# Optimization experiments

Measured on AMD Instinct MI355X. Metric: run time of the kernel, lower is better.

The kernel has to match this reference:

```python
import jax, jax.numpy as jnp
import numpy as np
from jax import lax

B, HI, WI, D = 8, 64, 64, 128
HO, WO = HI // 2, WI // 2
N_IN, N_OUT = HI * WI, HO * WO
NUM_ITERS = 3
EPS = 1e-6


def _build_indices(Ho, Wo):
    # replicates _build_q_and_in_idx: per coarse position, 9 relative offsets
    dys = np.repeat(np.arange(-1, 2), 3)
    dxs = np.tile(np.arange(-1, 2), 3)
    oy = np.arange(Ho)[:, None, None]
    ox = np.arange(Wo)[None, :, None]
    ny = oy + dys
    nx = ox + dxs
    valid = (ny >= 0) & (ny < Ho) & (nx >= 0) & (nx < Wo)  # (Ho,Wo,9)
    coarse = np.where(valid, ny * Wo + nx, 0)
    base = (oy * Wo + ox) * 9
    g9 = np.where(valid, base + np.arange(9), 0).reshape(-1, 9)
    c9 = coarse.reshape(-1, 9)
    q_idx = np.stack([np.tile(g9, (1, 4))] * 4)
    col_idx = np.stack([np.tile(c9, (1, 4))] * 4)
    in_idx = np.stack([np.tile(np.where(valid, coarse * 4 + h, 0).reshape(-1, 9), (1, 4)) for h in range(4)])
    return q_idx.astype(np.int32), in_idx.astype(np.int32), col_idx.astype(np.int32)


Q_IDX, IN_IDX, COL_IDX = _build_indices(HO, WO)
# NATTEN kernel-3 neighborhoods: window center clamped to stay in-bounds.
NY = np.clip(np.arange(HO) - 1, 0, HO - 3)[:, None] + np.arange(3)  # (HO,3)
NX = np.clip(np.arange(WO) - 1, 0, WO - 3)[:, None] + np.arange(3)  # (WO,3)


def _ln(x, g, b, eps=1e-5):
    mu = x.mean(-1, keepdims=True)
    var = ((x - mu) ** 2).mean(-1, keepdims=True)
    return (x - mu) * lax.rsqrt(var + eps) * g + b


def _forward(x, seed_w, wq, wk, wv, w1, b1, w2, b2, ln_in_g, ln_in_b, ln_out_g, ln_out_b, rpb, tau):
    ny, nx = jnp.asarray(NY), jnp.asarray(NX)
    q_idx = jnp.asarray(Q_IDX)

    def unfold(t):  # (B,HI,WI,D) -> (B,4,HO,WO,D); head = ky*2+kx (F.unfold order)
        return t.reshape(B, HO, 2, WO, 2, D).transpose(0, 2, 4, 1, 3, 5).reshape(B, 4, HO, WO, D)

    k = unfold((_ln(x, ln_in_g, ln_in_b) @ wk.T).reshape(B, HI, WI, D))
    v = unfold((x @ wv.T).reshape(B, HI, WI, D))
    k_n = k[:, :, ny][:, :, :, :, nx]  # (B,4,HO,3,WO,3,D)
    v_n = v[:, :, ny][:, :, :, :, nx]

    x_map = x.reshape(B, HI, WI, D).transpose(0, 3, 1, 2)
    seed = lax.conv_general_dilated(x_map, seed_w, (2, 2), ((1, 1), (1, 1)),
                                    dimension_numbers=('NCHW', 'OIHW', 'NCHW'))
    x_out = _ln(seed.reshape(B, D, N_OUT).transpose(0, 2, 1), ln_out_g, ln_out_b)

    scale = jnp.exp(tau)
    attn36 = a_col_h = None
    for _ in range(NUM_ITERS):
        q = (_ln(x_out, ln_out_g, ln_out_b) @ wq.T).reshape(B, HO, WO, D)
        # na2d_qk (q broadcast over the 4 heads) + relative position bias
        logits = jnp.einsum('byxd,bhykxld->bhyxkl', q, k_n).reshape(B, 4, HO, WO, 9) + rpb.reshape(1, 4, 1, 1, 9)
        attn = jax.nn.softmax(logits * scale, axis=-1) + EPS
        flat = attn.reshape(B, 4, N_OUT * 9)
        attn36 = jnp.take_along_axis(
            flat, jnp.broadcast_to(q_idx.reshape(1, 4, -1), (B, 4, N_OUT * 36)), axis=-1
        ).reshape(B, 4, N_OUT, 36)
        a_col_h = attn36 / (attn36.sum(axis=(1, 3), keepdims=True) + EPS)
        attn9 = a_col_h[..., :9].reshape(B, 4, HO, WO, 3, 3)
        # na2d_av then sum over heads
        updates = jnp.einsum('bhyxkl,bhykxld->byxd', attn9, v_n).reshape(B, N_OUT, D)
        x_out = x_out + updates
        h1 = jax.nn.gelu(x_out @ w1.T + b1, approximate=False)
        x_out = x_out + _ln(h1 @ w2.T + b2, ln_out_g, ln_out_b)
    return x_out, attn36, a_col_h


def setup_inputs() -> dict:
    key = jax.random.key(0)
    ks = jax.random.split(key, 8)
    n = lambda k, shape, s: jax.random.normal(k, shape, jnp.float32) * s
    D2 = 2 * D
    return {
        'x': jax.random.normal(ks[0], (B, N_IN, D), jnp.float32),
        'seed_w': n(ks[1], (D, D, 3, 3), (2.0 / (9 * D)) ** 0.5),
        'wq': n(ks[2], (D, D), D ** -0.5),
        'wk': n(ks[3], (D, D), D ** -0.5),
        'wv': n(ks[4], (D, D), D ** -0.5),
        'w1': n(ks[5], (D2, D), D ** -0.5),
        'b1': jnp.zeros((D2,), jnp.float32),
        'w2': n(ks[6], (D, D2), D2 ** -0.5),
        'b2': jnp.zeros((D,), jnp.float32),
        'ln_in_g': jnp.ones((D,), jnp.float32),
        'ln_in_b': jnp.zeros((D,), jnp.float32),
        'ln_out_g': jnp.ones((D,), jnp.float32),
        'ln_out_b': jnp.zeros((D,), jnp.float32),
        'rpb': n(ks[7], (4, 9), 0.02),
        'tau': jnp.float32(np.log(D ** -0.5)),
    }


def reference(x, seed_w, wq, wk, wv, w1, b1, w2, b2, ln_in_g, ln_in_b, ln_out_g, ln_out_b, rpb, tau):
    x_out, attn36, a_col_h = _forward(x, seed_w, wq, wk, wv, w1, b1, w2, b2,
                                      ln_in_g, ln_in_b, ln_out_g, ln_out_b, rpb, tau)
    # A_col: scatter_add over dim 1 -> A_col[b, in_idx[i,j], j] += a_col_h[b,i,j]
    rows = jnp.asarray(IN_IDX).reshape(4 * N_OUT, 36)
    cols = jnp.broadcast_to(jnp.arange(36), rows.shape)
    A_col = jnp.zeros((B, N_IN, N_OUT), x.dtype).at[:, rows, cols].add(a_col_h.reshape(B, 4 * N_OUT, 36))
    # A_row: scatter_add over dim 2 -> A_row[b, i, col_idx[i,j]] += attn36[b,i,j]
    ri = jnp.broadcast_to(jnp.arange(4 * N_OUT)[:, None], (4 * N_OUT, 36))
    A_row = jnp.zeros((B, N_IN, N_OUT), x.dtype).at[:, ri, jnp.asarray(COL_IDX).reshape(4 * N_OUT, 36)].add(
        attn36.reshape(B, 4 * N_OUT, 36))
    return x_out, A_row, A_col
```

## Files before the change

### kernel.cpp

```cpp
#include <hip/hip_runtime.h>
#include <hip/hip_bf16.h>
#include <math.h>

#define BB   8
#define HI_  64
#define WI_  64
#define DD   128
#define HO_  32
#define WO_  32
#define NIN  4096
#define NOUT 1024
#define LN_EPS 1e-5f
#define ATT_EPS 1e-6f

typedef short bf16x8 __attribute__((ext_vector_type(8)));
typedef float f32x4  __attribute__((ext_vector_type(4)));

__device__ __forceinline__ ushort f2bf(float f) {
    union { float f; unsigned u; } a; a.f = f;
    unsigned u = a.u;
    return (ushort)((u + 0x7FFFu + ((u >> 16) & 1u)) >> 16);
}
__device__ __forceinline__ float bf2f(ushort u) {
    union { unsigned u; float f; } a; a.u = ((unsigned)u) << 16;
    return a.f;
}

__global__ __launch_bounds__(256)
void wconvert_kernel(const float* __restrict__ wq, const float* __restrict__ wk,
                     const float* __restrict__ wv, const float* __restrict__ w1,
                     const float* __restrict__ w2, const float* __restrict__ sw,
                     ushort* __restrict__ dst)
{
    int i = blockIdx.x * 256 + threadIdx.x;
    float v;
    if (i < 16384)        v = wk[i];
    else if (i < 32768)   v = wv[i - 16384];
    else if (i < 49152)   v = wq[i - 32768];
    else if (i < 81920)   v = w1[i - 49152];
    else if (i < 114688)  v = w2[i - 81920];
    else {
        int j = i - 114688;
        int n = j / 1152;
        int rem = j - n * 1152;
        int tap = rem >> 7, di = rem & 127;
        v = sw[((size_t)(n * DD + di)) * 9 + tap];
    }
    dst[i] = f2bf(v);
}

__global__ __launch_bounds__(256)
void prep_kernel(const float* __restrict__ x, const ushort* __restrict__ wkb,
                 const ushort* __restrict__ wvb, const ushort* __restrict__ wcb,
                 const float* __restrict__ ligg, const float* __restrict__ libb,
                 const float* __restrict__ logg, const float* __restrict__ lobb,
                 ushort* __restrict__ kbuf, ushort* __restrict__ vbuf,
                 float* __restrict__ xout)
{
    __shared__ __align__(16) char arena[138752];
    const int tid = threadIdx.x;
    const int wid = tid >> 6, lane = tid & 63;
    const int lr = lane & 15, lk = (lane >> 4) << 3;

    if (blockIdx.x < 512) {
        float  (*xs)[132]   = (float  (*)[132])(arena);
        ushort (*Aln)[136]  = (ushort (*)[136])(arena + 33792);
        ushort (*Araw)[136] = (ushort (*)[136])(arena + 51200);
        ushort (*Bk)[136]   = (ushort (*)[136])(arena + 68608);
        ushort (*Bv)[136]   = (ushort (*)[136])(arena + 103424);
        float  (*rstat)[2]  = (float  (*)[2])(arena + 138240);
        const int row0 = blockIdx.x * 64;

        #pragma unroll
        for (int i = 0; i < 8; ++i) {
            int l = tid + i * 256;
            int r = l >> 5, c4 = (l & 31) << 2;
            float4 v = *(const float4*)(x + (size_t)(row0 + r) * DD + c4);
            *(float4*)&xs[r][c4] = v;
            ushort4 o; o.x = f2bf(v.x); o.y = f2bf(v.y); o.z = f2bf(v.z); o.w = f2bf(v.w);
            *(ushort4*)&Araw[r][c4] = o;
        }
        __syncthreads();
        {
            int r = tid >> 2, q = tid & 3;
            float s = 0.f, s2 = 0.f;
            #pragma unroll
            for (int c = 0; c < 32; ++c) { float v = xs[r][q * 32 + c]; s += v; s2 += v * v; }
            s += __shfl_down(s, 1, 64); s2 += __shfl_down(s2, 1, 64);
            s += __shfl_down(s, 2, 64); s2 += __shfl_down(s2, 2, 64);
            if (q == 0) {
                float mu = s * (1.f / DD);
                float var = s2 * (1.f / DD) - mu * mu;
                rstat[r][0] = mu; rstat[r][1] = rsqrtf(var + LN_EPS);
            }
        }
        __syncthreads();
        #pragma unroll
        for (int i = 0; i < 8; ++i) {
            int l = tid + i * 256;
            int r = l >> 5, c4 = (l & 31) << 2;
            float mu = rstat[r][0], rs = rstat[r][1];
            ushort4 o;
            o.x = f2bf((xs[r][c4 + 0] - mu) * rs * ligg[c4 + 0] + libb[c4 + 0]);
            o.y = f2bf((xs[r][c4 + 1] - mu) * rs * ligg[c4 + 1] + libb[c4 + 1]);
            o.z = f2bf((xs[r][c4 + 2] - mu) * rs * ligg[c4 + 2] + libb[c4 + 2]);
            o.w = f2bf((xs[r][c4 + 3] - mu) * rs * ligg[c4 + 3] + libb[c4 + 3]);
            *(ushort4*)&Aln[r][c4] = o;
        }
        #pragma unroll
        for (int i = 0; i < 8; ++i) {
            int l = tid + i * 256;
            int r = l >> 4, c8 = (l & 15) << 3;
            *(uint4*)&Bk[r][c8] = *(const uint4*)(wkb + (size_t)r * DD + c8);
            *(uint4*)&Bv[r][c8] = *(const uint4*)(wvb + (size_t)r * DD + c8);
        }
        __syncthreads();

        const int wm = (wid & 1) * 32, wn = (wid >> 1) * 64;
        f32x4 ak[2][4] = {}, av[2][4] = {};
        #pragma unroll
        for (int ks = 0; ks < 4; ++ks) {
            int kk = ks * 32 + lk;
            bf16x8 aL[2], aR[2];
            #pragma unroll
            for (int mi = 0; mi < 2; ++mi) {
                aL[mi] = *(const bf16x8*)&Aln[wm + mi * 16 + lr][kk];
                aR[mi] = *(const bf16x8*)&Araw[wm + mi * 16 + lr][kk];
            }
            #pragma unroll
            for (int ni = 0; ni < 4; ++ni) {
                bf16x8 bK = *(const bf16x8*)&Bk[wn + ni * 16 + lr][kk];
                bf16x8 bV = *(const bf16x8*)&Bv[wn + ni * 16 + lr][kk];
                #pragma unroll
                for (int mi = 0; mi < 2; ++mi) {
                    ak[mi][ni] = __builtin_amdgcn_mfma_f32_16x16x32_bf16(aL[mi], bK, ak[mi][ni], 0, 0, 0);
                    av[mi][ni] = __builtin_amdgcn_mfma_f32_16x16x32_bf16(aR[mi], bV, av[mi][ni], 0, 0, 0);
                }
            }
        }
        #pragma unroll
        for (int mi = 0; mi < 2; ++mi) {
            #pragma unroll
            for (int ni = 0; ni < 4; ++ni) {
                int n = wn + ni * 16 + (lane & 15);
                #pragma unroll
                for (int r = 0; r < 4; ++r) {
                    int m = row0 + wm + mi * 16 + ((lane >> 4) << 2) + r;
                    int b = m >> 12, pix = m & 4095;
                    int iy = pix >> 6, ix = pix & 63;
                    int h = ((iy & 1) << 1) | (ix & 1);
                    int cp = ((iy >> 1) << 5) | (ix >> 1);
                    size_t orow = ((size_t)(b * 4 + h) << 10) + cp;
                    kbuf[orow * DD + n] = f2bf(ak[mi][ni][r]);
                    vbuf[orow * DD + n] = f2bf(av[mi][ni][r]);
                }
            }
        }
    } else {
        ushort (*As)[72]   = (ushort (*)[72])(arena);
        ushort (*Bs)[72]   = (ushort (*)[72])(arena + 9216);
        float  (*es)[132]  = (float  (*)[132])(arena + 27648);
        float  (*rstat)[2] = (float  (*)[2])(arena + 61440);
        const int row0 = (blockIdx.x - 512) * 64;
        const int wm = (wid & 1) * 32, wn = (wid >> 1) * 64;
        f32x4 acc[2][4] = {};

        for (int k0 = 0; k0 < 1152; k0 += 64) {
            #pragma unroll
            for (int i = 0; i < 4; ++i) {
                int l = tid + i * 256;
                int r = l >> 4, c4 = (l & 15) << 2;
                int m = row0 + r;
                int b = m >> 10, p = m & 1023;
                int y = p >> 5, xx = p & 31;
                int kg = k0 + c4;
                int tap = kg >> 7, di = kg & 127;
                int ky = tap / 3, kx = tap - ky * 3;
                int iy = 2 * y + ky - 1, ix = 2 * xx + kx - 1;
                float4 v;
                if ((unsigned)iy < (unsigned)HI_ && (unsigned)ix < (unsigned)WI_)
                    v = *(const float4*)(x + ((size_t)b * NIN + iy * WI_ + ix) * DD + di);
                else v = make_float4(0.f, 0.f, 0.f, 0.f);
                ushort4 o; o.x = f2bf(v.x); o.y = f2bf(v.y); o.z = f2bf(v.z); o.w = f2bf(v.w);
                *(ushort4*)&As[r][c4] = o;
            }
            #pragma unroll
            for (int i = 0; i < 4; ++i) {
                int l = tid + i * 256;
                int r = l >> 3, c8 = (l & 7) << 3;
                *(uint4*)&Bs[r][c8] = *(const uint4*)(wcb + (size_t)r * 1152 + k0 + c8);
            }
            __syncthreads();
            #pragma unroll
            for (int ks = 0; ks < 2; ++ks) {
                int kk = ks * 32 + lk;
                bf16x8 aF[2];
                aF[0] = *(const bf16x8*)&As[wm + lr][kk];
                aF[1] = *(const bf16x8*)&As[wm + 16 + lr][kk];
                #pragma unroll
                for (int ni = 0; ni < 4; ++ni) {
                    bf16x8 bF = *(const bf16x8*)&Bs[wn + ni * 16 + lr][kk];
                    acc[0][ni] = __builtin_amdgcn_mfma_f32_16x16x32_bf16(aF[0], bF, acc[0][ni], 0, 0, 0);
                    acc[1][ni] = __builtin_amdgcn_mfma_f32_16x16x32_bf16(aF[1], bF, acc[1][ni], 0, 0, 0);
                }
            }
            __syncthreads();
        }
        #pragma unroll
        for (int mi = 0; mi < 2; ++mi)
            #pragma unroll
            for (int ni = 0; ni < 4; ++ni) {
                int n = wn + ni * 16 + (lane & 15);
                #pragma unroll
                for (int r = 0; r < 4; ++r)
                    es[wm + mi * 16 + ((lane >> 4) << 2) + r][n] = acc[mi][ni][r];
            }
        __syncthreads();
        {
            int r = tid >> 2, q = tid & 3;
            float s = 0.f, s2 = 0.f;
            #pragma unroll
            for (int c = 0; c < 32; ++c) { float v = es[r][q * 32 + c]; s += v; s2 += v * v; }
            s += __shfl_down(s, 1, 64); s2 += __shfl_down(s2, 1, 64);
            s += __shfl_down(s, 2, 64); s2 += __shfl_down(s2, 2, 64);
            if (q == 0) {
                float mu = s * (1.f / DD);
                float var = s2 * (1.f / DD) - mu * mu;
                rstat[r][0] = mu; rstat[r][1] = rsqrtf(var + LN_EPS);
            }
        }
        __syncthreads();
        #pragma unroll
        for (int i = 0; i < 8; ++i) {
            int l = tid + i * 256;
            int r = l >> 5, c4 = (l & 31) << 2;
            float mu = rstat[r][0], rs = rstat[r][1];
            float4 o;
            o.x = (es[r][c4 + 0] - mu) * rs * logg[c4 + 0] + lobb[c4 + 0];
            o.y = (es[r][c4 + 1] - mu) * rs * logg[c4 + 1] + lobb[c4 + 1];
            o.z = (es[r][c4 + 2] - mu) * rs * logg[c4 + 2] + lobb[c4 + 2];
            o.w = (es[r][c4 + 3] - mu) * rs * logg[c4 + 3] + lobb[c4 + 3];
            *(float4*)(xout + (size_t)(row0 + r) * DD + c4) = o;
        }
    }
}

template<int LAST>
__global__ __launch_bounds__(256)
void iter_kernel(float* __restrict__ xout, const ushort* __restrict__ kbuf,
                 const ushort* __restrict__ vbuf, const ushort* __restrict__ wqb,
                 const ushort* __restrict__ w1b, const ushort* __restrict__ w2b,
                 const float* __restrict__ b1, const float* __restrict__ b2,
                 const float* __restrict__ lg_, const float* __restrict__ lb_,
                 const float* __restrict__ rpb, const float* __restrict__ tau,
                 float* __restrict__ gbuf, float* __restrict__ denb,
                 float* __restrict__ out)
{
    const int bid = blockIdx.x;
    const int b = bid >> 6, cy = (bid >> 1) & 31, cx0 = (bid & 1) << 4;
    const int ry0 = min(max(cy - 1, 0), HO_ - 3);
    const int tid = threadIdx.x;
    const int wid = tid >> 6, lane = tid & 63;
    const int lr = lane & 15, lk = (lane >> 4) << 3;

    __shared__ float  xsf[17][132];
    __shared__ ushort Aq[32][136];
    __shared__ ushort qs[17][136];
    __shared__ float  rstat[17][2];
    __shared__ float  lgp[16][36];
    __shared__ float  lg0[36];
    __shared__ float  sm0[4];
    __shared__ float  den[16];
    __shared__ float  hsum[16][4];
    __shared__ ushort h1s[16][264];
    __shared__ float  es[16][132];

    for (int l = tid; l < 544; l += 256) {
        int r = l >> 5, c4 = (l & 31) << 2;
        int g = b * NOUT + (r < 16 ? cy * 32 + cx0 + r : 0);
        *(float4*)&xsf[r][c4] = *(const float4*)(xout + (size_t)g * DD + c4);
    }
    __syncthreads();
    if (tid < 68) {
        int r = tid >> 2, q = tid & 3;
        float s = 0.f, s2 = 0.f;
        #pragma unroll
        for (int c = 0; c < 32; ++c) { float v = xsf[r][q * 32 + c]; s += v; s2 += v * v; }
        s += __shfl_down(s, 1, 64); s2 += __shfl_down(s2, 1, 64);
        s += __shfl_down(s, 2, 64); s2 += __shfl_down(s2, 2, 64);
        if (q == 0) {
            float mu = s * (1.f / DD);
            float var = s2 * (1.f / DD) - mu * mu;
            rstat[r][0] = mu; rstat[r][1] = rsqrtf(var + LN_EPS);
        }
    }
    __syncthreads();
    for (int l = tid; l < 544; l += 256) {
        int r = l >> 5, c4 = (l & 31) << 2;
        float mu = rstat[r][0], rs = rstat[r][1];
        ushort4 o;
        o.x = f2bf((xsf[r][c4 + 0] - mu) * rs * lg_[c4 + 0] + lb_[c4 + 0]);
        o.y = f2bf((xsf[r][c4 + 1] - mu) * rs * lg_[c4 + 1] + lb_[c4 + 1]);
        o.z = f2bf((xsf[r][c4 + 2] - mu) * rs * lg_[c4 + 2] + lb_[c4 + 2]);
        o.w = f2bf((xsf[r][c4 + 3] - mu) * rs * lg_[c4 + 3] + lb_[c4 + 3]);
        *(ushort4*)&Aq[r][c4] = o;
    }
    for (int l = tid; l < 480; l += 256) {
        int r = 17 + (l >> 5), c4 = (l & 31) << 2;
        ushort4 z; z.x = 0; z.y = 0; z.z = 0; z.w = 0;
        *(ushort4*)&Aq[r][c4] = z;
    }
    __syncthreads();

    {
        const int wn = wid * 32;
        f32x4 acc[2][2] = {};
        #pragma unroll
        for (int ks = 0; ks < 4; ++ks) {
            int kk = ks * 32 + lk;
            bf16x8 aF[2];
            aF[0] = *(const bf16x8*)&Aq[lr][kk];
            aF[1] = *(const bf16x8*)&Aq[16 + lr][kk];
            #pragma unroll
            for (int ni = 0; ni < 2; ++ni) {
                bf16x8 bF = *(const bf16x8*)(wqb + (size_t)(wn + ni * 16 + lr) * DD + kk);
                acc[0][ni] = __builtin_amdgcn_mfma_f32_16x16x32_bf16(aF[0], bF, acc[0][ni], 0, 0, 0);
                acc[1][ni] = __builtin_amdgcn_mfma_f32_16x16x32_bf16(aF[1], bF, acc[1][ni], 0, 0, 0);
            }
        }
        #pragma unroll
        for (int mi = 0; mi < 2; ++mi)
            #pragma unroll
            for (int ni = 0; ni < 2; ++ni) {
                int n = wn + ni * 16 + (lane & 15);
                #pragma unroll
                for (int r = 0; r < 4; ++r) {
                    int m = mi * 16 + ((lane >> 4) << 2) + r;
                    if (m < 17) qs[m][n] = f2bf(acc[mi][ni][r]);
                }
            }
    }
    __syncthreads();

    for (int task = tid; task < 612; task += 256) {
        const ushort *kp, *qp;
        int cl = 0, h, jj;
        if (task < 576) {
            cl = task / 36; int t2 = task - cl * 36;
            h = t2 / 9; jj = t2 - h * 9;
            int ky = jj / 3, kx = jj - ky * 3;
            int c = cx0 + cl;
            int nx = min(max(c - 1, 0), WO_ - 3) + kx;
            kp = kbuf + (((size_t)(b * 4 + h) << 10) + (ry0 + ky) * 32 + nx) * DD;
            qp = &qs[cl][0];
        } else {
            int t2 = task - 576;
            h = t2 / 9; jj = t2 - h * 9;
            int ky = jj / 3, kx = jj - ky * 3;
            kp = kbuf + (((size_t)(b * 4 + h) << 10) + ky * 32 + kx) * DD;
            qp = &qs[16][0];
        }
        float s = 0.f;
        #pragma unroll
        for (int d = 0; d < 128; d += 8) {
            uint4 ku = *(const uint4*)(kp + d);
            uint4 qu = *(const uint4*)(qp + d);
            const ushort* kk2 = (const ushort*)&ku;
            const ushort* qq2 = (const ushort*)&qu;
            #pragma unroll
            for (int t = 0; t < 8; ++t) s += bf2f(kk2[t]) * bf2f(qq2[t]);
        }
        if (task < 576) lgp[cl][h * 9 + jj] = s;
        else            lg0[task - 576] = s;
    }
    __syncthreads();

    if (tid < 68) {
        float scale = expf(tau[0]);
        int h; const float* lptr; int cl = 0;
        if (tid < 64) { cl = tid >> 2; h = tid & 3; lptr = &lgp[cl][h * 9]; }
        else          { h = tid - 64; lptr = &lg0[h * 9]; }
        float tmpv[9], mx = -1e30f;
        #pragma unroll
        for (int jj = 0; jj < 9; ++jj) {
            float v = (lptr[jj] + rpb[h * 9 + jj]) * scale;
            tmpv[jj] = v; mx = fmaxf(mx, v);
        }
        float ss = 0.f;
        #pragma unroll
        for (int jj = 0; jj < 9; ++jj) { tmpv[jj] = expf(tmpv[jj] - mx); ss += tmpv[jj]; }
        float inv = 1.f / ss;
        if (tid < 64) {
            #pragma unroll
            for (int jj = 0; jj < 9; ++jj) lgp[cl][h * 9 + jj] = tmpv[jj] * inv + ATT_EPS;
        } else sm0[h] = tmpv[0] * inv + ATT_EPS;
    }
    __syncthreads();

    if (tid < 64) {
        int cl = tid >> 2, h = tid & 3;
        int c = cx0 + cl;
        float s = 0.f, gv[9];
        #pragma unroll
        for (int jj = 0; jj < 9; ++jj) {
            int dy = jj / 3 - 1, dx = jj % 3 - 1;
            bool valid = ((unsigned)(cy + dy) < (unsigned)HO_) && ((unsigned)(c + dx) < (unsigned)WO_);
            float v = valid ? lgp[cl][h * 9 + jj] : sm0[h];
            gv[jj] = v; s += v;
        }
        float* gp = gbuf + (((size_t)(b * 4 + h) << 10) + cy * 32 + c) * 9;
        #pragma unroll
        for (int jj = 0; jj < 9; ++jj) { gp[jj] = gv[jj]; lgp[cl][h * 9 + jj] = gv[jj]; }
        hsum[cl][h] = s;
    }
    __syncthreads();
    if (tid < 16) {
        float dd = 4.f * (hsum[tid][0] + hsum[tid][1] + hsum[tid][2] + hsum[tid][3]) + ATT_EPS;
        den[tid] = 1.f / dd;
        denb[b * NOUT + cy * 32 + cx0 + tid] = dd;
    }
    __syncthreads();
    if (tid < 64) {
        int cl = tid >> 2, h = tid & 3;
        float inv = den[cl];
        #pragma unroll
        for (int jj = 0; jj < 9; ++jj) lgp[cl][h * 9 + jj] *= inv;
    }
    __syncthreads();

    {
        int cl = tid >> 4, d0 = (tid & 15) << 3;
        int c = cx0 + cl;
        int rx0 = min(max(c - 1, 0), WO_ - 3);
        float acc[8] = {};
        #pragma unroll
        for (int h = 0; h < 4; ++h)
            #pragma unroll
            for (int jj = 0; jj < 9; ++jj) {
                float cf = lgp[cl][h * 9 + jj];
                int ky = jj / 3, kx = jj - ky * 3;
                const ushort* vp = vbuf + (((size_t)(b * 4 + h) << 10) + (ry0 + ky) * 32 + rx0 + kx) * DD + d0;
                uint4 v0 = *(const uint4*)(vp);
                const ushort* vs0 = (const ushort*)&v0;
                #pragma unroll
                for (int t = 0; t < 8; ++t) acc[t] += cf * bf2f(vs0[t]);
            }
        #pragma unroll
        for (int t = 0; t < 8; t += 4) {
            float4 o = *(float4*)&xsf[cl][d0 + t];
            o.x += acc[t]; o.y += acc[t + 1]; o.z += acc[t + 2]; o.w += acc[t + 3];
            *(float4*)&xsf[cl][d0 + t] = o;
        }
    }
    __syncthreads();

    for (int l = tid; l < 512; l += 256) {
        int r = l >> 5, c4 = (l & 31) << 2;
        ushort4 o;
        o.x = f2bf(xsf[r][c4 + 0]); o.y = f2bf(xsf[r][c4 + 1]);
        o.z = f2bf(xsf[r][c4 + 2]); o.w = f2bf(xsf[r][c4 + 3]);
        *(ushort4*)&Aq[r][c4] = o;
    }
    __syncthreads();
    {
        const int wn = wid * 64;
        f32x4 acc[4] = {};
        #pragma unroll
        for (int ks = 0; ks < 4; ++ks) {
            int kk = ks * 32 + lk;
            bf16x8 a0 = *(const bf16x8*)&Aq[lr][kk];
            #pragma unroll
            for (int ni = 0; ni < 4; ++ni) {
                bf16x8 bF = *(const bf16x8*)(w1b + (size_t)(wn + ni * 16 + lr) * DD + kk);
                acc[ni] = __builtin_amdgcn_mfma_f32_16x16x32_bf16(a0, bF, acc[ni], 0, 0, 0);
            }
        }
        #pragma unroll
        for (int ni = 0; ni < 4; ++ni) {
            int n = wn + ni * 16 + (lane & 15);
            float bv = b1[n];
            #pragma unroll
            for (int r = 0; r < 4; ++r) {
                int m = ((lane >> 4) << 2) + r;
                float v = acc[ni][r] + bv;
                v = 0.5f * v * (1.f + erff(v * 0.70710678118654752f));
                h1s[m][n] = f2bf(v);
            }
        }
    }
    __syncthreads();

    {
        const int wn = wid * 32;
        f32x4 acc[2] = {};
        #pragma unroll
        for (int ks = 0; ks < 8; ++ks) {
            int kk = ks * 32 + lk;
            bf16x8 a0 = *(const bf16x8*)&h1s[lr][kk];
            #pragma unroll
            for (int ni = 0; ni < 2; ++ni) {
                bf16x8 bF = *(const bf16x8*)(w2b + (size_t)(wn + ni * 16 + lr) * 256 + kk);
                acc[ni] = __builtin_amdgcn_mfma_f32_16x16x32_bf16(a0, bF, acc[ni], 0, 0, 0);
            }
        }
        #pragma unroll
        for (int ni = 0; ni < 2; ++ni) {
            int n = wn + ni * 16 + (lane & 15);
            float bv = b2[n];
            #pragma unroll
            for (int r = 0; r < 4; ++r)
                es[((lane >> 4) << 2) + r][n] = acc[ni][r] + bv;
        }
    }
    __syncthreads();
    if (tid < 128) {
        int r = tid >> 3, qq = tid & 7;
        float s = 0.f, s2 = 0.f;
        #pragma unroll
        for (int c = 0; c < 16; ++c) { float v = es[r][qq * 16 + c]; s += v; s2 += v * v; }
        s += __shfl_down(s, 1, 64); s2 += __shfl_down(s2, 1, 64);
        s += __shfl_down(s, 2, 64); s2 += __shfl_down(s2, 2, 64);
        s += __shfl_down(s, 4, 64); s2 += __shfl_down(s2, 4, 64);
        if (qq == 0) {
            float mu = s * (1.f / DD);
            float var = s2 * (1.f / DD) - mu * mu;
            rstat[r][0] = mu; rstat[r][1] = rsqrtf(var + LN_EPS);
        }
    }
    __syncthreads();
    for (int l = tid; l < 512; l += 256) {
        int r = l >> 5, c4 = (l & 31) << 2;
        float mu = rstat[r][0], rs = rstat[r][1];
        size_t off = ((size_t)(b * NOUT + cy * 32 + cx0 + r)) * DD + c4;
        float4 o;
        o.x = xsf[r][c4 + 0] + (es[r][c4 + 0] - mu) * rs * lg_[c4 + 0] + lb_[c4 + 0];
        o.y = xsf[r][c4 + 1] + (es[r][c4 + 1] - mu) * rs * lg_[c4 + 1] + lb_[c4 + 1];
        o.z = xsf[r][c4 + 2] + (es[r][c4 + 2] - mu) * rs * lg_[c4 + 2] + lb_[c4 + 2];
        o.w = xsf[r][c4 + 3] + (es[r][c4 + 3] - mu) * rs * lg_[c4 + 3] + lb_[c4 + 3];
        *(float4*)(xout + off) = o;
        if (LAST) *(float4*)(out + off) = o;
    }
}

__global__ __launch_bounds__(256)
void arowcol_kernel(const float* __restrict__ gbuf, const float* __restrict__ denb,
                    float* __restrict__ Arow, float* __restrict__ Acol)
{
    const int tid = threadIdx.x;
    __shared__ int   cols[9];
    __shared__ float vals[9];
    __shared__ float wred[9][4];
    if (blockIdx.x < 32768) {
        const int bi = blockIdx.x;
        const int b = bi >> 12, i = bi & 4095;
        const int h = i >> 10, p = i & 1023;
        const int cy = p >> 5, cx = p & 31;
        if (tid < 9) {
            int dy = tid / 3 - 1, dx = tid % 3 - 1;
            bool valid = ((unsigned)(cy + dy) < (unsigned)HO_) && ((unsigned)(cx + dx) < (unsigned)WO_);
            cols[tid] = valid ? (cy + dy) * WO_ + (cx + dx) : 0;
            vals[tid] = 4.f * gbuf[(((size_t)(b * 4 + h) << 10) + p) * 9 + tid];
        }
        __syncthreads();
        float* row = Arow + (size_t)bi * NOUT;
        #pragma unroll
        for (int cc = 0; cc < 4; ++cc) {
            int c = cc * 256 + tid;
            float acc = 0.f;
            #pragma unroll
            for (int jj = 0; jj < 9; ++jj)
                if (cols[jj] == c) acc += vals[jj];
            row[c] = acc;
        }
    } else {
        const int br = blockIdx.x - 32768;
        const int b = br >> 12, r = br & 4095;
        const int h = r & 3, coarse = r >> 2;
        const int cy = coarse >> 5, cx = coarse & 31;
        if (tid < 9) {
            int dy = tid / 3 - 1, dx = tid % 3 - 1;
            int py = cy - dy, px = cx - dx;
            float v = 0.f;
            if ((unsigned)py < (unsigned)HO_ && (unsigned)px < (unsigned)WO_) {
                int p = py * WO_ + px;
                v = gbuf[(((size_t)(b * 4 + h) << 10) + p) * 9 + tid] / denb[b * NOUT + p];
            }
            vals[tid] = v;
        }
        if (r == 0) {
            float part[9] = {};
            for (int p = tid; p < NOUT; p += 256) {
                float invd = 1.f / denb[b * NOUT + p];
                int py = p >> 5, px = p & 31;
                #pragma unroll
                for (int jj = 0; jj < 9; ++jj) {
                    int dy = jj / 3 - 1, dx = jj % 3 - 1;
                    bool valid = ((unsigned)(py + dy) < (unsigned)HO_) && ((unsigned)(px + dx) < (unsigned)WO_);
                    if (!valid) part[jj] += invd;
                }
            }
            #pragma unroll
            for (int jj = 0; jj < 9; ++jj) {
                float s = part[jj];
                #pragma unroll
                for (int o = 32; o > 0; o >>= 1) s += __shfl_down(s, o, 64);
                if ((tid & 63) == 0) wred[jj][tid >> 6] = s;
            }
            __syncthreads();
            if (tid < 9) {
                float s = wred[tid][0] + wred[tid][1] + wred[tid][2] + wred[tid][3];
                float H = 0.f;
                for (int h2 = 0; h2 < 4; ++h2)
                    H += gbuf[(((size_t)(b * 4 + h2)) << 10) * 9];
                vals[tid] += H * s;
            }
        }
        __syncthreads();
        float* row = Acol + (size_t)br * NOUT;
        #pragma unroll
        for (int cc = 0; cc < 4; ++cc) {
            int c = cc * 256 + tid;
            row[c] = (c < 36) ? vals[c % 9] : 0.f;
        }
    }
}

extern "C" void kernel_launch(void* const* d_in, const int* in_sizes, int n_in,
                              void* d_out, int out_size, void* d_ws, size_t ws_size,
                              hipStream_t stream)
{
    const float* x        = (const float*)d_in[0];
    const float* seed_w   = (const float*)d_in[1];
    const float* wq       = (const float*)d_in[2];
    const float* wk       = (const float*)d_in[3];
    const float* wv       = (const float*)d_in[4];
    const float* w1       = (const float*)d_in[5];
    const float* b1       = (const float*)d_in[6];
    const float* w2       = (const float*)d_in[7];
    const float* b2       = (const float*)d_in[8];
    const float* ln_in_g  = (const float*)d_in[9];
    const float* ln_in_b  = (const float*)d_in[10];
    const float* ln_out_g = (const float*)d_in[11];
    const float* ln_out_b = (const float*)d_in[12];
    const float* rpb      = (const float*)d_in[13];
    const float* tau      = (const float*)d_in[14];

    float* out  = (float*)d_out;
    float* Arow = out + (size_t)BB * NOUT * DD;
    float* Acol = Arow + (size_t)BB * NIN * NOUT;

    float* ws    = (float*)d_ws;
    float* xout  = ws;
    float* gbuf  = xout + (size_t)BB * NOUT * DD;
    float* denb  = gbuf + (size_t)BB * 4 * NOUT * 9;
    ushort* wb   = (ushort*)(denb + BB * NOUT);
    ushort* wkb  = wb;
    ushort* wvb  = wb + 16384;
    ushort* wqb  = wb + 32768;
    ushort* w1b  = wb + 49152;
    ushort* w2b  = wb + 81920;
    ushort* wcb  = wb + 114688;

    ushort* kbuf = (ushort*)Arow;
    ushort* vbuf = kbuf + (size_t)4194304;

    wconvert_kernel<<<1024, 256, 0, stream>>>(wq, wk, wv, w1, w2, seed_w, wb);
    prep_kernel<<<640, 256, 0, stream>>>(x, wkb, wvb, wcb, ln_in_g, ln_in_b,
                                         ln_out_g, ln_out_b, kbuf, vbuf, xout);

    for (int it = 0; it < 3; ++it) {
        if (it < 2)
            iter_kernel<0><<<BB * HO_ * 2, 256, 0, stream>>>(
                xout, kbuf, vbuf, wqb, w1b, w2b, b1, b2, ln_out_g, ln_out_b,
                rpb, tau, gbuf, denb, out);
        else
            iter_kernel<1><<<BB * HO_ * 2, 256, 0, stream>>>(
                xout, kbuf, vbuf, wqb, w1b, w2b, b1, b2, ln_out_g, ln_out_b,
                rpb, tau, gbuf, denb, out);
    }

    arowcol_kernel<<<2 * BB * NIN, 256, 0, stream>>>(gbuf, denb, Arow, Acol);
}
```

Measured before the change: 190.1 us.

## Shrink prep LDS footprint and double iter_kernel block size to 512 threads

In prep_kernel the LayerNorm row statistics are now computed from registers with warp shuffles, and the K/V weight tiles are read straight from global memory, so the LDS arena drops from about 138KB to about 62KB and more blocks can be resident. iter_kernel now launches with 512 threads and splits each MFMA stage's N-work across twice as many waves. The per-head denominator is reduced with 4-lane shuffles, which removes the hsum/den shared arrays and two barriers. In exchange, prep_kernel re-reads weights from global or L2 inside the MFMA loop, and each wave in iter_kernel has less work to hide latency.

```diff
diff --git a/kernel.cpp b/kernel.cpp
--- a/kernel.cpp
+++ b/kernel.cpp
@@ -57,38 +57,34 @@
                  ushort* __restrict__ kbuf, ushort* __restrict__ vbuf,
                  float* __restrict__ xout)
 {
-    __shared__ __align__(16) char arena[138752];
+    __shared__ __align__(16) char arena[62208];
     const int tid = threadIdx.x;
     const int wid = tid >> 6, lane = tid & 63;
     const int lr = lane & 15, lk = (lane >> 4) << 3;
 
     if (blockIdx.x < 512) {
-        float  (*xs)[132]   = (float  (*)[132])(arena);
-        ushort (*Aln)[136]  = (ushort (*)[136])(arena + 33792);
-        ushort (*Araw)[136] = (ushort (*)[136])(arena + 51200);
-        ushort (*Bk)[136]   = (ushort (*)[136])(arena + 68608);
-        ushort (*Bv)[136]   = (ushort (*)[136])(arena + 103424);
-        float  (*rstat)[2]  = (float  (*)[2])(arena + 138240);
+        ushort (*Araw)[136] = (ushort (*)[136])(arena);
+        ushort (*Aln)[136]  = (ushort (*)[136])(arena + 17408);
+        float  (*rstat)[2]  = (float  (*)[2])(arena + 34816);
         const int row0 = blockIdx.x * 64;
 
+        float4 xv[8];
         #pragma unroll
         for (int i = 0; i < 8; ++i) {
             int l = tid + i * 256;
             int r = l >> 5, c4 = (l & 31) << 2;
             float4 v = *(const float4*)(x + (size_t)(row0 + r) * DD + c4);
-            *(float4*)&xs[r][c4] = v;
+            xv[i] = v;
             ushort4 o; o.x = f2bf(v.x); o.y = f2bf(v.y); o.z = f2bf(v.z); o.w = f2bf(v.w);
             *(ushort4*)&Araw[r][c4] = o;
-        }
-        __syncthreads();
-        {
-            int r = tid >> 2, q = tid & 3;
-            float s = 0.f, s2 = 0.f;
-            #pragma unroll
-            for (int c = 0; c < 32; ++c) { float v = xs[r][q * 32 + c]; s += v; s2 += v * v; }
-            s += __shfl_down(s, 1, 64); s2 += __shfl_down(s2, 1, 64);
-            s += __shfl_down(s, 2, 64); s2 += __shfl_down(s2, 2, 64);
-            if (q == 0) {
+            float s  = v.x + v.y + v.z + v.w;
+            float s2 = v.x * v.x + v.y * v.y + v.z * v.z + v.w * v.w;
+            #pragma unroll
+            for (int o2 = 16; o2 > 0; o2 >>= 1) {
+                s  += __shfl_down(s,  o2, 32);
+                s2 += __shfl_down(s2, o2, 32);
+            }
+            if ((tid & 31) == 0) {
                 float mu = s * (1.f / DD);
                 float var = s2 * (1.f / DD) - mu * mu;
                 rstat[r][0] = mu; rstat[r][1] = rsqrtf(var + LN_EPS);
@@ -100,19 +96,13 @@
             int l = tid + i * 256;
             int r = l >> 5, c4 = (l & 31) << 2;
             float mu = rstat[r][0], rs = rstat[r][1];
+            float4 v = xv[i];
             ushort4 o;
-            o.x = f2bf((xs[r][c4 + 0] - mu) * rs * ligg[c4 + 0] + libb[c4 + 0]);
-            o.y = f2bf((xs[r][c4 + 1] - mu) * rs * ligg[c4 + 1] + libb[c4 + 1]);
-            o.z = f2bf((xs[r][c4 + 2] - mu) * rs * ligg[c4 + 2] + libb[c4 + 2]);
-            o.w = f2bf((xs[r][c4 + 3] - mu) * rs * ligg[c4 + 3] + libb[c4 + 3]);
+            o.x = f2bf((v.x - mu) * rs * ligg[c4 + 0] + libb[c4 + 0]);
+            o.y = f2bf((v.y - mu) * rs * ligg[c4 + 1] + libb[c4 + 1]);
+            o.z = f2bf((v.z - mu) * rs * ligg[c4 + 2] + libb[c4 + 2]);
+            o.w = f2bf((v.w - mu) * rs * ligg[c4 + 3] + libb[c4 + 3]);
             *(ushort4*)&Aln[r][c4] = o;
-        }
-        #pragma unroll
-        for (int i = 0; i < 8; ++i) {
-            int l = tid + i * 256;
-            int r = l >> 4, c8 = (l & 15) << 3;
-            *(uint4*)&Bk[r][c8] = *(const uint4*)(wkb + (size_t)r * DD + c8);
-            *(uint4*)&Bv[r][c8] = *(const uint4*)(wvb + (size_t)r * DD + c8);
         }
         __syncthreads();
 
@@ -129,8 +119,8 @@
             }
             #pragma unroll
             for (int ni = 0; ni < 4; ++ni) {
-                bf16x8 bK = *(const bf16x8*)&Bk[wn + ni * 16 + lr][kk];
-                bf16x8 bV = *(const bf16x8*)&Bv[wn + ni * 16 + lr][kk];
+                bf16x8 bK = *(const bf16x8*)(wkb + (size_t)(wn + ni * 16 + lr) * DD + kk);
+                bf16x8 bV = *(const bf16x8*)(wvb + (size_t)(wn + ni * 16 + lr) * DD + kk);
                 #pragma unroll
                 for (int mi = 0; mi < 2; ++mi) {
                     ak[mi][ni] = __builtin_amdgcn_mfma_f32_16x16x32_bf16(aL[mi], bK, ak[mi][ni], 0, 0, 0);
@@ -246,7 +236,7 @@
 }
 
 template<int LAST>
-__global__ __launch_bounds__(256)
+__global__ __launch_bounds__(512, 4)
 void iter_kernel(float* __restrict__ xout, const ushort* __restrict__ kbuf,
                  const ushort* __restrict__ vbuf, const ushort* __restrict__ wqb,
                  const ushort* __restrict__ w1b, const ushort* __restrict__ w2b,
@@ -270,12 +260,10 @@
     __shared__ float  lgp[16][36];
     __shared__ float  lg0[36];
     __shared__ float  sm0[4];
-    __shared__ float  den[16];
-    __shared__ float  hsum[16][4];
     __shared__ ushort h1s[16][264];
     __shared__ float  es[16][132];
 
-    for (int l = tid; l < 544; l += 256) {
+    for (int l = tid; l < 544; l += 512) {
         int r = l >> 5, c4 = (l & 31) << 2;
         int g = b * NOUT + (r < 16 ? cy * 32 + cx0 + r : 0);
         *(float4*)&xsf[r][c4] = *(const float4*)(xout + (size_t)g * DD + c4);
@@ -295,7 +283,7 @@
         }
     }
     __syncthreads();
-    for (int l = tid; l < 544; l += 256) {
+    for (int l = tid; l < 544; l += 512) {
         int r = l >> 5, c4 = (l & 31) << 2;
         float mu = rstat[r][0], rs = rstat[r][1];
         ushort4 o;
@@ -305,7 +293,7 @@
         o.w = f2bf((xsf[r][c4 + 3] - mu) * rs * lg_[c4 + 3] + lb_[c4 + 3]);
         *(ushort4*)&Aq[r][c4] = o;
     }
-    for (int l = tid; l < 480; l += 256) {
+    for (int l = tid; l < 480; l += 512) {
         int r = 17 + (l >> 5), c4 = (l & 31) << 2;
         ushort4 z; z.x = 0; z.y = 0; z.z = 0; z.w = 0;
         *(ushort4*)&Aq[r][c4] = z;
@@ -313,36 +301,29 @@
     __syncthreads();
 
     {
-        const int wn = wid * 32;
-        f32x4 acc[2][2] = {};
+        const int wn = wid * 16;
+        f32x4 acc[2] = {};
         #pragma unroll
         for (int ks = 0; ks < 4; ++ks) {
             int kk = ks * 32 + lk;
-            bf16x8 aF[2];
-            aF[0] = *(const bf16x8*)&Aq[lr][kk];
-            aF[1] = *(const bf16x8*)&Aq[16 + lr][kk];
-            #pragma unroll
-            for (int ni = 0; ni < 2; ++ni) {
-                bf16x8 bF = *(const bf16x8*)(wqb + (size_t)(wn + ni * 16 + lr) * DD + kk);
-                acc[0][ni] = __builtin_amdgcn_mfma_f32_16x16x32_bf16(aF[0], bF, acc[0][ni], 0, 0, 0);
-                acc[1][ni] = __builtin_amdgcn_mfma_f32_16x16x32_bf16(aF[1], bF, acc[1][ni], 0, 0, 0);
-            }
-        }
+            bf16x8 aF0 = *(const bf16x8*)&Aq[lr][kk];
+            bf16x8 aF1 = *(const bf16x8*)&Aq[16 + lr][kk];
+            bf16x8 bF = *(const bf16x8*)(wqb + (size_t)(wn + lr) * DD + kk);
+            acc[0] = __builtin_amdgcn_mfma_f32_16x16x32_bf16(aF0, bF, acc[0], 0, 0, 0);
+            acc[1] = __builtin_amdgcn_mfma_f32_16x16x32_bf16(aF1, bF, acc[1], 0, 0, 0);
+        }
+        int n = wn + (lane & 15);
         #pragma unroll
         for (int mi = 0; mi < 2; ++mi)
             #pragma unroll
-            for (int ni = 0; ni < 2; ++ni) {
-                int n = wn + ni * 16 + (lane & 15);
-                #pragma unroll
-                for (int r = 0; r < 4; ++r) {
-                    int m = mi * 16 + ((lane >> 4) << 2) + r;
-                    if (m < 17) qs[m][n] = f2bf(acc[mi][ni][r]);
-                }
-            }
-    }
-    __syncthreads();
-
-    for (int task = tid; task < 612; task += 256) {
+            for (int r = 0; r < 4; ++r) {
+                int m = mi * 16 + ((lane >> 4) << 2) + r;
+                if (m < 17) qs[m][n] = f2bf(acc[mi][r]);
+            }
+    }
+    __syncthreads();
+
+    for (int task = tid; task < 612; task += 512) {
         const ushort *kp, *qp;
         int cl = 0, h, jj;
         if (task < 576) {
@@ -361,7 +342,7 @@
             qp = &qs[16][0];
         }
         float s = 0.f;
-        #pragma unroll
+        #pragma unroll 4
         for (int d = 0; d < 128; d += 8) {
             uint4 ku = *(const uint4*)(kp + d);
             uint4 qu = *(const uint4*)(qp + d);
@@ -408,31 +389,26 @@
             float v = valid ? lgp[cl][h * 9 + jj] : sm0[h];
             gv[jj] = v; s += v;
         }
+        float tot = s;
+        tot += __shfl_xor(tot, 1, 4);
+        tot += __shfl_xor(tot, 2, 4);
+        float dd = 4.f * tot + ATT_EPS;
+        if (h == 0) denb[b * NOUT + cy * 32 + cx0 + cl] = dd;
+        float inv = 1.f / dd;
         float* gp = gbuf + (((size_t)(b * 4 + h) << 10) + cy * 32 + c) * 9;
         #pragma unroll
-        for (int jj = 0; jj < 9; ++jj) { gp[jj] = gv[jj]; lgp[cl][h * 9 + jj] = gv[jj]; }
-        hsum[cl][h] = s;
-    }
-    __syncthreads();
-    if (tid < 16) {
-        float dd = 4.f * (hsum[tid][0] + hsum[tid][1] + hsum[tid][2] + hsum[tid][3]) + ATT_EPS;
-        den[tid] = 1.f / dd;
-        denb[b * NOUT + cy * 32 + cx0 + tid] = dd;
-    }
-    __syncthreads();
-    if (tid < 64) {
-        int cl = tid >> 2, h = tid & 3;
-        float inv = den[cl];
-        #pragma unroll
-        for (int jj = 0; jj < 9; ++jj) lgp[cl][h * 9 + jj] *= inv;
+        for (int jj = 0; jj < 9; ++jj) {
+            gp[jj] = gv[jj];
+            lgp[cl][h * 9 + jj] = gv[jj] * inv;
+        }
     }
     __syncthreads();
 
     {
-        int cl = tid >> 4, d0 = (tid & 15) << 3;
+        int cl = tid >> 5, d0 = (tid & 31) << 2;
         int c = cx0 + cl;
         int rx0 = min(max(c - 1, 0), WO_ - 3);
-        float acc[8] = {};
+        float acc4[4] = {};
         #pragma unroll
         for (int h = 0; h < 4; ++h)
             #pragma unroll
@@ -440,21 +416,19 @@
                 float cf = lgp[cl][h * 9 + jj];
                 int ky = jj / 3, kx = jj - ky * 3;
                 const ushort* vp = vbuf + (((size_t)(b * 4 + h) << 10) + (ry0 + ky) * 32 + rx0 + kx) * DD + d0;
-                uint4 v0 = *(const uint4*)(vp);
+                uint2 v0 = *(const uint2*)(vp);
                 const ushort* vs0 = (const ushort*)&v0;
                 #pragma unroll
-                for (int t = 0; t < 8; ++t) acc[t] += cf * bf2f(vs0[t]);
-            }
-        #pragma unroll
-        for (int t = 0; t < 8; t += 4) {
-            float4 o = *(float4*)&xsf[cl][d0 + t];
-            o.x += acc[t]; o.y += acc[t + 1]; o.z += acc[t + 2]; o.w += acc[t + 3];
-            *(float4*)&xsf[cl][d0 + t] = o;
-        }
-    }
-    __syncthreads();
-
-    for (int l = tid; l < 512; l += 256) {
+                for (int t = 0; t < 4; ++t) acc4[t] += cf * bf2f(vs0[t]);
+            }
+        float4 o = *(float4*)&xsf[cl][d0];
+        o.x += acc4[0]; o.y += acc4[1]; o.z += acc4[2]; o.w += acc4[3];
+        *(float4*)&xsf[cl][d0] = o;
+    }
+    __syncthreads();
+
+    {
+        int l = tid;
         int r = l >> 5, c4 = (l & 31) << 2;
         ushort4 o;
         o.x = f2bf(xsf[r][c4 + 0]); o.y = f2bf(xsf[r][c4 + 1]);
@@ -463,20 +437,20 @@
     }
     __syncthreads();
     {
-        const int wn = wid * 64;
-        f32x4 acc[4] = {};
+        const int wn = wid * 32;
+        f32x4 acc[2] = {};
         #pragma unroll
         for (int ks = 0; ks < 4; ++ks) {
             int kk = ks * 32 + lk;
             bf16x8 a0 = *(const bf16x8*)&Aq[lr][kk];
             #pragma unroll
-            for (int ni = 0; ni < 4; ++ni) {
+            for (int ni = 0; ni < 2; ++ni) {
                 bf16x8 bF = *(const bf16x8*)(w1b + (size_t)(wn + ni * 16 + lr) * DD + kk);
                 acc[ni] = __builtin_amdgcn_mfma_f32_16x16x32_bf16(a0, bF, acc[ni], 0, 0, 0);
             }
         }
         #pragma unroll
-        for (int ni = 0; ni < 4; ++ni) {
+        for (int ni = 0; ni < 2; ++ni) {
             int n = wn + ni * 16 + (lane & 15);
             float bv = b1[n];
             #pragma unroll
@@ -491,26 +465,20 @@
     __syncthreads();
 
     {
-        const int wn = wid * 32;
-        f32x4 acc[2] = {};
+        const int wn = wid * 16;
+        f32x4 acc = {};
         #pragma unroll
         for (int ks = 0; ks < 8; ++ks) {
             int kk = ks * 32 + lk;
             bf16x8 a0 = *(const bf16x8*)&h1s[lr][kk];
-            #pragma unroll
-            for (int ni = 0; ni < 2; ++ni) {
-                bf16x8 bF = *(const bf16x8*)(w2b + (size_t)(wn + ni * 16 + lr) * 256 + kk);
-                acc[ni] = __builtin_amdgcn_mfma_f32_16x16x32_bf16(a0, bF, acc[ni], 0, 0, 0);
-            }
-        }
-        #pragma unroll
-        for (int ni = 0; ni < 2; ++ni) {
-            int n = wn + ni * 16 + (lane & 15);
-            float bv = b2[n];
-            #pragma unroll
-            for (int r = 0; r < 4; ++r)
-                es[((lane >> 4) << 2) + r][n] = acc[ni][r] + bv;
-        }
+            bf16x8 bF = *(const bf16x8*)(w2b + (size_t)(wn + lr) * 256 + kk);
+            acc = __builtin_amdgcn_mfma_f32_16x16x32_bf16(a0, bF, acc, 0, 0, 0);
+        }
+        int n = wn + (lane & 15);
+        float bv = b2[n];
+        #pragma unroll
+        for (int r = 0; r < 4; ++r)
+            es[((lane >> 4) << 2) + r][n] = acc[r] + bv;
     }
     __syncthreads();
     if (tid < 128) {
@@ -528,7 +496,8 @@
         }
     }
     __syncthreads();
-    for (int l = tid; l < 512; l += 256) {
+    {
+        int l = tid;
         int r = l >> 5, c4 = (l & 31) << 2;
         float mu = rstat[r][0], rs = rstat[r][1];
         size_t off = ((size_t)(b * NOUT + cy * 32 + cx0 + r)) * DD + c4;
@@ -670,11 +639,11 @@
 
     for (int it = 0; it < 3; ++it) {
         if (it < 2)
-            iter_kernel<0><<<BB * HO_ * 2, 256, 0, stream>>>(
+            iter_kernel<0><<<BB * HO_ * 2, 512, 0, stream>>>(
                 xout, kbuf, vbuf, wqb, w1b, w2b, b1, b2, ln_out_g, ln_out_b,
                 rpb, tau, gbuf, denb, out);
         else
-            iter_kernel<1><<<BB * HO_ * 2, 256, 0, stream>>>(
+            iter_kernel<1><<<BB * HO_ * 2, 512, 0, stream>>>(
                 xout, kbuf, vbuf, wqb, w1b, w2b, b1, b2, ln_out_g, ln_out_b,
                 rpb, tau, gbuf, denb, out);
     }
```

After: 193.6 us. About the same (+1.9%).
